# Performance work log

Measured on AMD Instinct MI355X. Metric: run time of the kernel, lower is better.

## Reference

```python
import jax, jax.numpy as jnp
import numpy as np

MD = 2        # max_displacement
STRIDE2 = 2   # displacement grid stride -> shifts in {-2, 0, 2}


def conv3x3_same(x, w):
    # x: [B,C,H,W], w: [O,I,3,3], stride 1, padding 1, no bias
    return jax.lax.conv_general_dilated(
        x, w, window_strides=(1, 1), padding=((1, 1), (1, 1)),
        dimension_numbers=("NCHW", "OIHW", "NCHW"))


def correlation(f1, f2):
    # FlowNet-style correlation, kernel_size=1: for each displacement (dy,dx)
    # in {-MD..MD step STRIDE2}^2, per-pixel channel dot product of f1 with
    # shifted f2, normalized by C (sumelems = kernel_size^2 * C).
    B, C, H, W = f1.shape
    f2p = jnp.pad(f2, ((0, 0), (0, 0), (MD, MD), (MD, MD)))
    outs = []
    for dy in range(-MD, MD + 1, STRIDE2):
        for dx in range(-MD, MD + 1, STRIDE2):
            f2s = f2p[:, :, MD + dy:MD + dy + H, MD + dx:MD + dx + W]
            outs.append(jnp.mean(f1 * f2s, axis=1))  # [B,H,W]
    return jnp.stack(outs, axis=1)  # [B, 9, H, W]


def setup_inputs() -> dict:
    key = jax.random.key(0)
    k1, k2, k3 = jax.random.split(key, 3)
    B, C, H, W = 16, 3, 512, 512
    x1 = jax.random.normal(k1, (B, C, H, W), dtype=jnp.float32)
    x2 = jax.random.normal(k2, (B, C, H, W), dtype=jnp.float32)
    # conv1: Conv2d(3, 3, kernel_size=3, bias=False); kaiming-ish scale
    fan_in = C * 3 * 3
    conv_w = jax.random.normal(k3, (3, C, 3, 3), dtype=jnp.float32) * np.float32(np.sqrt(2.0 / fan_in))
    return {"x1": x1, "x2": x2, "conv_w": conv_w}


def reference(x1, x2, conv_w):
    f1 = conv3x3_same(x1, conv_w)
    f2 = conv3x3_same(x2, conv_w)
    return correlation(f1, f2)  # [B, 9, H, W]
```

## Files before the change

### kernel.cpp

```cpp
#include <hip/hip_runtime.h>


#define HH 512
#define WW 512
#define TS 32
#define X2R 38
#define X2S 40
#define X1R 34
#define X1S 36
#define F2R 36
#define F2S 40
#define N2 (3*X2R*X2S)
#define NF (3*F2R*F2S)
#define NC2 (3*X2R*(X2S/4))
#define NC1 (3*X1R*(X1S/4))

typedef const __attribute__((address_space(1))) void* gas_ptr;
typedef __attribute__((address_space(3))) void* las_ptr;
typedef float f32x4 __attribute__((ext_vector_type(4)));

__global__ __launch_bounds__(256)
void flownetc_fused_kernel(const float* __restrict__ x1,
                           const float* __restrict__ x2,
                           const float* __restrict__ cw,
                           float* __restrict__ out) {
  __shared__ __align__(16) float s_x2[N2];
  __shared__ __align__(16) float s_ov[NF];

  const int tid = threadIdx.x;
  const int bid = blockIdx.x;
  const int f   = (bid & 7) * 512 + (bid >> 3);
  const int ox0 = (f & 15) * TS;
  const int oy0 = ((f >> 4) & 15) * TS;
  const int bi  = f >> 8;

  const float* x2b = x2 + (size_t)bi * 3 * HH * WW;
  const float* x1b = x1 + (size_t)bi * 3 * HH * WW;

  for (int q = tid; q < NC2; q += 256) {
    const int colq = q % (X2S / 4);
    const int rp   = q / (X2S / 4);
    const int r    = rp % X2R;
    const int c    = rp / X2R;
    const int gy   = oy0 - 3 + r;
    const int gx0  = ox0 - 3 + colq * 4;
    const float* src = x2b + (size_t)(c * HH + gy) * WW + gx0;
    if ((unsigned)gy < HH && (unsigned)gx0 <= (WW - 4)) {
      __builtin_amdgcn_global_load_lds((gas_ptr)src,
          (las_ptr)(s_x2 + ((q & ~63) << 2)), 16, 0, 0);
    } else {
      const bool rowok = (unsigned)gy < HH;
      float4 v;
      v.x = (rowok && (unsigned)(gx0 + 0) < WW) ? src[0] : 0.f;
      v.y = (rowok && (unsigned)(gx0 + 1) < WW) ? src[1] : 0.f;
      v.z = (rowok && (unsigned)(gx0 + 2) < WW) ? src[2] : 0.f;
      v.w = (rowok && (unsigned)(gx0 + 3) < WW) ? src[3] : 0.f;
      *reinterpret_cast<float4*>(&s_x2[q * 4]) = v;
    }
  }
  for (int q = tid; q < NC1; q += 256) {
    const int colq = q % (X1S / 4);
    const int rp   = q / (X1S / 4);
    const int r    = rp % X1R;
    const int c    = rp / X1R;
    const int gy   = oy0 - 1 + r;
    const int gx0  = ox0 - 1 + colq * 4;
    const float* src = x1b + (size_t)(c * HH + gy) * WW + gx0;
    if ((unsigned)gy < HH && (unsigned)gx0 <= (WW - 4)) {
      __builtin_amdgcn_global_load_lds((gas_ptr)src,
          (las_ptr)(s_ov + ((q & ~63) << 2)), 16, 0, 0);
    } else {
      const bool rowok = (unsigned)gy < HH;
      float4 v;
      v.x = (rowok && (unsigned)(gx0 + 0) < WW) ? src[0] : 0.f;
      v.y = (rowok && (unsigned)(gx0 + 1) < WW) ? src[1] : 0.f;
      v.z = (rowok && (unsigned)(gx0 + 2) < WW) ? src[2] : 0.f;
      v.w = (rowok && (unsigned)(gx0 + 3) < WW) ? src[3] : 0.f;
      *reinterpret_cast<float4*>(&s_ov[q * 4]) = v;
    }
  }
  __syncthreads();

  auto f2unit = [&](int r, int col0, float acc[3][4]) {
    #pragma unroll
    for (int co = 0; co < 3; ++co)
      #pragma unroll
      for (int j = 0; j < 4; ++j) acc[co][j] = 0.f;
    #pragma unroll
    for (int ci = 0; ci < 3; ++ci) {
      float win[3][6];
      #pragma unroll
      for (int ky = 0; ky < 3; ++ky) {
        const float* base = &s_x2[(ci * X2R + r + ky) * X2S + col0];
        const float4 a  = *reinterpret_cast<const float4*>(base);
        const float2 b2 = *reinterpret_cast<const float2*>(base + 4);
        win[ky][0] = a.x; win[ky][1] = a.y; win[ky][2] = a.z; win[ky][3] = a.w;
        win[ky][4] = b2.x; win[ky][5] = b2.y;
      }
      #pragma unroll
      for (int co = 0; co < 3; ++co)
        #pragma unroll
        for (int ky = 0; ky < 3; ++ky)
          #pragma unroll
          for (int kx = 0; kx < 3; ++kx) {
            const float w = cw[((co * 3 + ci) * 3 + ky) * 3 + kx];
            #pragma unroll
            for (int j = 0; j < 4; ++j)
              acc[co][j] += w * win[ky][j + kx];
          }
    }
    const int gy = oy0 - 2 + r;
    #pragma unroll
    for (int j = 0; j < 4; ++j) {
      const int gx = ox0 - 2 + col0 + j;
      if (!((unsigned)gy < HH && (unsigned)gx < WW)) {
        acc[0][j] = 0.f; acc[1][j] = 0.f; acc[2][j] = 0.f;
      }
    }
  };

  const int r0   = tid >> 3;
  const int c0   = (tid & 7) << 2;
  float acc0[3][4];
  f2unit(r0, c0, acc0);
  float acc1[3][4];
  int r1 = 0, c1 = 0;
  if (tid < 68) {
    if (tid < 36) { r1 = 32 + tid / 9; c1 = (tid % 9) * 4; }
    else          { r1 = tid - 36;     c1 = 32; }
    f2unit(r1, c1, acc1);
  }

  const int py  = tid >> 3;
  const int px0 = (tid & 7) << 2;
  float f1r[3][4] = {};
  #pragma unroll
  for (int ci = 0; ci < 3; ++ci) {
    float win[3][6];
    #pragma unroll
    for (int ky = 0; ky < 3; ++ky) {
      const float* base = &s_ov[(ci * X1R + py + ky) * X1S + px0];
      const float4 a  = *reinterpret_cast<const float4*>(base);
      const float2 b2 = *reinterpret_cast<const float2*>(base + 4);
      win[ky][0] = a.x; win[ky][1] = a.y; win[ky][2] = a.z; win[ky][3] = a.w;
      win[ky][4] = b2.x; win[ky][5] = b2.y;
    }
    #pragma unroll
    for (int co = 0; co < 3; ++co)
      #pragma unroll
      for (int ky = 0; ky < 3; ++ky)
        #pragma unroll
        for (int kx = 0; kx < 3; ++kx) {
          const float w = cw[((co * 3 + ci) * 3 + ky) * 3 + kx];
          #pragma unroll
          for (int j = 0; j < 4; ++j)
            f1r[co][j] += w * win[ky][j + kx];
        }
  }
  #pragma unroll
  for (int co = 0; co < 3; ++co)
    #pragma unroll
    for (int j = 0; j < 4; ++j)
      f1r[co][j] *= (1.f / 3.f);
  __syncthreads();

  #pragma unroll
  for (int co = 0; co < 3; ++co)
    *reinterpret_cast<float4*>(&s_ov[(co * F2R + r0) * F2S + c0]) =
        make_float4(acc0[co][0], acc0[co][1], acc0[co][2], acc0[co][3]);
  if (tid < 68) {
    #pragma unroll
    for (int co = 0; co < 3; ++co)
      *reinterpret_cast<float4*>(&s_ov[(co * F2R + r1) * F2S + c1]) =
          make_float4(acc1[co][0], acc1[co][1], acc1[co][2], acc1[co][3]);
  }
  __syncthreads();

  float* outp = out + ((size_t)bi * 9 * HH + (oy0 + py)) * WW + ox0 + px0;
  #pragma unroll
  for (int dyi = 0; dyi < 3; ++dyi) {
    float rv[3][8];
    #pragma unroll
    for (int c = 0; c < 3; ++c) {
      const float* base = &s_ov[(c * F2R + py + dyi * 2) * F2S + px0];
      const float4 a = *reinterpret_cast<const float4*>(base);
      const float4 b = *reinterpret_cast<const float4*>(base + 4);
      rv[c][0] = a.x; rv[c][1] = a.y; rv[c][2] = a.z; rv[c][3] = a.w;
      rv[c][4] = b.x; rv[c][5] = b.y; rv[c][6] = b.z; rv[c][7] = b.w;
    }
    #pragma unroll
    for (int dxi = 0; dxi < 3; ++dxi) {
      const int s = dxi * 2;
      f32x4 o;
      o.x = f1r[0][0]*rv[0][s+0] + f1r[1][0]*rv[1][s+0] + f1r[2][0]*rv[2][s+0];
      o.y = f1r[0][1]*rv[0][s+1] + f1r[1][1]*rv[1][s+1] + f1r[2][1]*rv[2][s+1];
      o.z = f1r[0][2]*rv[0][s+2] + f1r[1][2]*rv[1][s+2] + f1r[2][2]*rv[2][s+2];
      o.w = f1r[0][3]*rv[0][s+3] + f1r[1][3]*rv[1][s+3] + f1r[2][3]*rv[2][s+3];
      __builtin_nontemporal_store(o,
          reinterpret_cast<f32x4*>(outp + (size_t)(dyi * 3 + dxi) * HH * WW));
    }
  }
}

extern "C" void kernel_launch(void* const* d_in, const int* in_sizes, int n_in,
                              void* d_out, int out_size, void* d_ws, size_t ws_size,
                              hipStream_t stream) {
  const float* x1 = (const float*)d_in[0];
  const float* x2 = (const float*)d_in[1];
  const float* cw = (const float*)d_in[2];
  float* out = (float*)d_out;

  flownetc_fused_kernel<<<dim3(4096), 256, 0, stream>>>(x1, x2, cw, out);
}
```

Baseline: 58.16 us.

## Process two vertical tiles per block and prefetch next x2 tile during store

Each block now handles two stacked 32x32 tiles, halving the grid. The x2 halo for the second tile is loaded asynchronously into LDS while the first tile's correlation outputs are computed and written, and the second f1 staging is overlapped with the f2 convolution. The aim is to hide global load latency behind the output stores. The cost is fewer blocks in flight, more barriers per block, and no reduction in halo traffic.

```diff
diff --git a/kernel.cpp b/kernel.cpp
--- a/kernel.cpp
+++ b/kernel.cpp
@@ -29,59 +29,67 @@
 
   const int tid = threadIdx.x;
   const int bid = blockIdx.x;
-  const int f   = (bid & 7) * 512 + (bid >> 3);
+  const int f   = (bid & 7) * 256 + (bid >> 3);
   const int ox0 = (f & 15) * TS;
-  const int oy0 = ((f >> 4) & 15) * TS;
-  const int bi  = f >> 8;
+  const int oyA = ((f >> 4) & 7) * 64;
+  const int bi  = f >> 7;
 
   const float* x2b = x2 + (size_t)bi * 3 * HH * WW;
   const float* x1b = x1 + (size_t)bi * 3 * HH * WW;
 
-  for (int q = tid; q < NC2; q += 256) {
-    const int colq = q % (X2S / 4);
-    const int rp   = q / (X2S / 4);
-    const int r    = rp % X2R;
-    const int c    = rp / X2R;
-    const int gy   = oy0 - 3 + r;
-    const int gx0  = ox0 - 3 + colq * 4;
-    const float* src = x2b + (size_t)(c * HH + gy) * WW + gx0;
-    if ((unsigned)gy < HH && (unsigned)gx0 <= (WW - 4)) {
-      __builtin_amdgcn_global_load_lds((gas_ptr)src,
-          (las_ptr)(s_x2 + ((q & ~63) << 2)), 16, 0, 0);
-    } else {
-      const bool rowok = (unsigned)gy < HH;
-      float4 v;
-      v.x = (rowok && (unsigned)(gx0 + 0) < WW) ? src[0] : 0.f;
-      v.y = (rowok && (unsigned)(gx0 + 1) < WW) ? src[1] : 0.f;
-      v.z = (rowok && (unsigned)(gx0 + 2) < WW) ? src[2] : 0.f;
-      v.w = (rowok && (unsigned)(gx0 + 3) < WW) ? src[3] : 0.f;
-      *reinterpret_cast<float4*>(&s_x2[q * 4]) = v;
-    }
-  }
-  for (int q = tid; q < NC1; q += 256) {
-    const int colq = q % (X1S / 4);
-    const int rp   = q / (X1S / 4);
-    const int r    = rp % X1R;
-    const int c    = rp / X1R;
-    const int gy   = oy0 - 1 + r;
-    const int gx0  = ox0 - 1 + colq * 4;
-    const float* src = x1b + (size_t)(c * HH + gy) * WW + gx0;
-    if ((unsigned)gy < HH && (unsigned)gx0 <= (WW - 4)) {
-      __builtin_amdgcn_global_load_lds((gas_ptr)src,
-          (las_ptr)(s_ov + ((q & ~63) << 2)), 16, 0, 0);
-    } else {
-      const bool rowok = (unsigned)gy < HH;
-      float4 v;
-      v.x = (rowok && (unsigned)(gx0 + 0) < WW) ? src[0] : 0.f;
-      v.y = (rowok && (unsigned)(gx0 + 1) < WW) ? src[1] : 0.f;
-      v.z = (rowok && (unsigned)(gx0 + 2) < WW) ? src[2] : 0.f;
-      v.w = (rowok && (unsigned)(gx0 + 3) < WW) ? src[3] : 0.f;
-      *reinterpret_cast<float4*>(&s_ov[q * 4]) = v;
-    }
-  }
-  __syncthreads();
-
-  auto f2unit = [&](int r, int col0, float acc[3][4]) {
+  const int py  = tid >> 3;
+  const int px0 = (tid & 7) << 2;
+  const int r0  = py;
+  const int c0  = px0;
+
+  auto stage_x2 = [&](int oy0) {
+    for (int q = tid; q < NC2; q += 256) {
+      const int colq = q % (X2S / 4);
+      const int rp   = q / (X2S / 4);
+      const int r    = rp % X2R;
+      const int c    = rp / X2R;
+      const int gy   = oy0 - 3 + r;
+      const int gx0  = ox0 - 3 + colq * 4;
+      const float* src = x2b + (size_t)(c * HH + gy) * WW + gx0;
+      if ((unsigned)gy < HH && (unsigned)gx0 <= (WW - 4)) {
+        __builtin_amdgcn_global_load_lds((gas_ptr)src,
+            (las_ptr)(s_x2 + ((q & ~63) << 2)), 16, 0, 0);
+      } else {
+        const bool rowok = (unsigned)gy < HH;
+        float4 v;
+        v.x = (rowok && (unsigned)(gx0 + 0) < WW) ? src[0] : 0.f;
+        v.y = (rowok && (unsigned)(gx0 + 1) < WW) ? src[1] : 0.f;
+        v.z = (rowok && (unsigned)(gx0 + 2) < WW) ? src[2] : 0.f;
+        v.w = (rowok && (unsigned)(gx0 + 3) < WW) ? src[3] : 0.f;
+        *reinterpret_cast<float4*>(&s_x2[q * 4]) = v;
+      }
+    }
+  };
+  auto stage_x1 = [&](int oy0) {
+    for (int q = tid; q < NC1; q += 256) {
+      const int colq = q % (X1S / 4);
+      const int rp   = q / (X1S / 4);
+      const int r    = rp % X1R;
+      const int c    = rp / X1R;
+      const int gy   = oy0 - 1 + r;
+      const int gx0  = ox0 - 1 + colq * 4;
+      const float* src = x1b + (size_t)(c * HH + gy) * WW + gx0;
+      if ((unsigned)gy < HH && (unsigned)gx0 <= (WW - 4)) {
+        __builtin_amdgcn_global_load_lds((gas_ptr)src,
+            (las_ptr)(s_ov + ((q & ~63) << 2)), 16, 0, 0);
+      } else {
+        const bool rowok = (unsigned)gy < HH;
+        float4 v;
+        v.x = (rowok && (unsigned)(gx0 + 0) < WW) ? src[0] : 0.f;
+        v.y = (rowok && (unsigned)(gx0 + 1) < WW) ? src[1] : 0.f;
+        v.z = (rowok && (unsigned)(gx0 + 2) < WW) ? src[2] : 0.f;
+        v.w = (rowok && (unsigned)(gx0 + 3) < WW) ? src[3] : 0.f;
+        *reinterpret_cast<float4*>(&s_ov[q * 4]) = v;
+      }
+    }
+  };
+
+  auto f2unit = [&](int oy0, int r, int col0, float acc[3][4]) {
     #pragma unroll
     for (int co = 0; co < 3; ++co)
       #pragma unroll
@@ -119,87 +127,121 @@
     }
   };
 
-  const int r0   = tid >> 3;
-  const int c0   = (tid & 7) << 2;
-  float acc0[3][4];
-  f2unit(r0, c0, acc0);
-  float acc1[3][4];
   int r1 = 0, c1 = 0;
-  if (tid < 68) {
-    if (tid < 36) { r1 = 32 + tid / 9; c1 = (tid % 9) * 4; }
-    else          { r1 = tid - 36;     c1 = 32; }
-    f2unit(r1, c1, acc1);
-  }
-
-  const int py  = tid >> 3;
-  const int px0 = (tid & 7) << 2;
-  float f1r[3][4] = {};
-  #pragma unroll
-  for (int ci = 0; ci < 3; ++ci) {
-    float win[3][6];
-    #pragma unroll
-    for (int ky = 0; ky < 3; ++ky) {
-      const float* base = &s_ov[(ci * X1R + py + ky) * X1S + px0];
-      const float4 a  = *reinterpret_cast<const float4*>(base);
-      const float2 b2 = *reinterpret_cast<const float2*>(base + 4);
-      win[ky][0] = a.x; win[ky][1] = a.y; win[ky][2] = a.z; win[ky][3] = a.w;
-      win[ky][4] = b2.x; win[ky][5] = b2.y;
-    }
-    #pragma unroll
-    for (int co = 0; co < 3; ++co)
-      #pragma unroll
-      for (int ky = 0; ky < 3; ++ky)
+  if (tid < 36)      { r1 = 32 + tid / 9; c1 = (tid % 9) * 4; }
+  else if (tid < 68) { r1 = tid - 36;     c1 = 32; }
+
+  auto f2compute = [&](int oy0, float a0[3][4], float a1[3][4]) {
+    f2unit(oy0, r0, c0, a0);
+    if (tid < 68) f2unit(oy0, r1, c1, a1);
+  };
+  auto f2write = [&](float a0[3][4], float a1[3][4]) {
+    #pragma unroll
+    for (int co = 0; co < 3; ++co)
+      *reinterpret_cast<float4*>(&s_ov[(co * F2R + r0) * F2S + c0]) =
+          make_float4(a0[co][0], a0[co][1], a0[co][2], a0[co][3]);
+    if (tid < 68) {
+      #pragma unroll
+      for (int co = 0; co < 3; ++co)
+        *reinterpret_cast<float4*>(&s_ov[(co * F2R + r1) * F2S + c1]) =
+            make_float4(a1[co][0], a1[co][1], a1[co][2], a1[co][3]);
+    }
+  };
+
+  auto f1compute = [&](float f1r[3][4]) {
+    #pragma unroll
+    for (int co = 0; co < 3; ++co)
+      #pragma unroll
+      for (int j = 0; j < 4; ++j) f1r[co][j] = 0.f;
+    #pragma unroll
+    for (int ci = 0; ci < 3; ++ci) {
+      float win[3][6];
+      #pragma unroll
+      for (int ky = 0; ky < 3; ++ky) {
+        const float* base = &s_ov[(ci * X1R + py + ky) * X1S + px0];
+        const float4 a  = *reinterpret_cast<const float4*>(base);
+        const float2 b2 = *reinterpret_cast<const float2*>(base + 4);
+        win[ky][0] = a.x; win[ky][1] = a.y; win[ky][2] = a.z; win[ky][3] = a.w;
+        win[ky][4] = b2.x; win[ky][5] = b2.y;
+      }
+      #pragma unroll
+      for (int co = 0; co < 3; ++co)
         #pragma unroll
-        for (int kx = 0; kx < 3; ++kx) {
-          const float w = cw[((co * 3 + ci) * 3 + ky) * 3 + kx];
+        for (int ky = 0; ky < 3; ++ky)
           #pragma unroll
-          for (int j = 0; j < 4; ++j)
-            f1r[co][j] += w * win[ky][j + kx];
-        }
-  }
-  #pragma unroll
-  for (int co = 0; co < 3; ++co)
-    #pragma unroll
-    for (int j = 0; j < 4; ++j)
-      f1r[co][j] *= (1.f / 3.f);
-  __syncthreads();
-
-  #pragma unroll
-  for (int co = 0; co < 3; ++co)
-    *reinterpret_cast<float4*>(&s_ov[(co * F2R + r0) * F2S + c0]) =
-        make_float4(acc0[co][0], acc0[co][1], acc0[co][2], acc0[co][3]);
-  if (tid < 68) {
-    #pragma unroll
-    for (int co = 0; co < 3; ++co)
-      *reinterpret_cast<float4*>(&s_ov[(co * F2R + r1) * F2S + c1]) =
-          make_float4(acc1[co][0], acc1[co][1], acc1[co][2], acc1[co][3]);
-  }
-  __syncthreads();
-
-  float* outp = out + ((size_t)bi * 9 * HH + (oy0 + py)) * WW + ox0 + px0;
-  #pragma unroll
-  for (int dyi = 0; dyi < 3; ++dyi) {
-    float rv[3][8];
-    #pragma unroll
-    for (int c = 0; c < 3; ++c) {
-      const float* base = &s_ov[(c * F2R + py + dyi * 2) * F2S + px0];
-      const float4 a = *reinterpret_cast<const float4*>(base);
-      const float4 b = *reinterpret_cast<const float4*>(base + 4);
-      rv[c][0] = a.x; rv[c][1] = a.y; rv[c][2] = a.z; rv[c][3] = a.w;
-      rv[c][4] = b.x; rv[c][5] = b.y; rv[c][6] = b.z; rv[c][7] = b.w;
-    }
-    #pragma unroll
-    for (int dxi = 0; dxi < 3; ++dxi) {
-      const int s = dxi * 2;
-      f32x4 o;
-      o.x = f1r[0][0]*rv[0][s+0] + f1r[1][0]*rv[1][s+0] + f1r[2][0]*rv[2][s+0];
-      o.y = f1r[0][1]*rv[0][s+1] + f1r[1][1]*rv[1][s+1] + f1r[2][1]*rv[2][s+1];
-      o.z = f1r[0][2]*rv[0][s+2] + f1r[1][2]*rv[1][s+2] + f1r[2][2]*rv[2][s+2];
-      o.w = f1r[0][3]*rv[0][s+3] + f1r[1][3]*rv[1][s+3] + f1r[2][3]*rv[2][s+3];
-      __builtin_nontemporal_store(o,
-          reinterpret_cast<f32x4*>(outp + (size_t)(dyi * 3 + dxi) * HH * WW));
-    }
-  }
+          for (int kx = 0; kx < 3; ++kx) {
+            const float w = cw[((co * 3 + ci) * 3 + ky) * 3 + kx];
+            #pragma unroll
+            for (int j = 0; j < 4; ++j)
+              f1r[co][j] += w * win[ky][j + kx];
+          }
+    }
+    #pragma unroll
+    for (int co = 0; co < 3; ++co)
+      #pragma unroll
+      for (int j = 0; j < 4; ++j)
+        f1r[co][j] *= (1.f / 3.f);
+  };
+
+  auto corr_store = [&](int oy0, float f1r[3][4]) {
+    float* outp = out + ((size_t)bi * 9 * HH + (oy0 + py)) * WW + ox0 + px0;
+    #pragma unroll
+    for (int dyi = 0; dyi < 3; ++dyi) {
+      float rv[3][8];
+      #pragma unroll
+      for (int c = 0; c < 3; ++c) {
+        const float* base = &s_ov[(c * F2R + py + dyi * 2) * F2S + px0];
+        const float4 a = *reinterpret_cast<const float4*>(base);
+        const float4 b = *reinterpret_cast<const float4*>(base + 4);
+        rv[c][0] = a.x; rv[c][1] = a.y; rv[c][2] = a.z; rv[c][3] = a.w;
+        rv[c][4] = b.x; rv[c][5] = b.y; rv[c][6] = b.z; rv[c][7] = b.w;
+      }
+      #pragma unroll
+      for (int dxi = 0; dxi < 3; ++dxi) {
+        const int s = dxi * 2;
+        f32x4 o;
+        o.x = f1r[0][0]*rv[0][s+0] + f1r[1][0]*rv[1][s+0] + f1r[2][0]*rv[2][s+0];
+        o.y = f1r[0][1]*rv[0][s+1] + f1r[1][1]*rv[1][s+1] + f1r[2][1]*rv[2][s+1];
+        o.z = f1r[0][2]*rv[0][s+2] + f1r[1][2]*rv[1][s+2] + f1r[2][2]*rv[2][s+2];
+        o.w = f1r[0][3]*rv[0][s+3] + f1r[1][3]*rv[1][s+3] + f1r[2][3]*rv[2][s+3];
+        __builtin_nontemporal_store(o,
+            reinterpret_cast<f32x4*>(outp + (size_t)(dyi * 3 + dxi) * HH * WW));
+      }
+    }
+  };
+
+  float acc0[3][4], acc1[3][4], f1r[3][4];
+
+  stage_x2(oyA);
+  stage_x1(oyA);
+  __syncthreads();
+
+  f2compute(oyA, acc0, acc1);
+  f1compute(f1r);
+  __syncthreads();
+
+  stage_x2(oyA + TS);
+  f2write(acc0, acc1);
+  asm volatile("s_waitcnt lgkmcnt(0)" ::: "memory");
+  __builtin_amdgcn_s_barrier();
+  __builtin_amdgcn_sched_barrier(0);
+
+  corr_store(oyA, f1r);
+  __syncthreads();
+
+  stage_x1(oyA + TS);
+  f2compute(oyA + TS, acc0, acc1);
+  __syncthreads();
+
+  f1compute(f1r);
+  __syncthreads();
+
+  f2write(acc0, acc1);
+  asm volatile("s_waitcnt lgkmcnt(0)" ::: "memory");
+  __builtin_amdgcn_s_barrier();
+  __builtin_amdgcn_sched_barrier(0);
+
+  corr_store(oyA + TS, f1r);
 }
 
 extern "C" void kernel_launch(void* const* d_in, const int* in_sizes, int n_in,
@@ -210,5 +252,5 @@
   const float* cw = (const float*)d_in[2];
   float* out = (float*)d_out;
 
-  flownetc_fused_kernel<<<dim3(4096), 256, 0, stream>>>(x1, x2, cw, out);
+  flownetc_fused_kernel<<<dim3(2048), 256, 0, stream>>>(x1, x2, cw, out);
 }
```

Measured after the change: 67.10 us. 15.4% more time.
